# Kernel tuning notes

Hardware: AMD Instinct MI355X
Metric: run time of the kernel (lower is better)

The kernel has to match this reference:

```python
import jax, jax.numpy as jnp
import numpy as np

D_MODEL = 128
NUM_HEADS = 8
DEPTH = D_MODEL // NUM_HEADS
NEG = -1e9


def _dense_params(key, d_in, d_out):
    kw, kb = jax.random.split(key)
    # Glorot-uniform like keras Dense default
    lim = np.sqrt(6.0 / (d_in + d_out))
    w = jax.random.uniform(kw, (d_in, d_out), jnp.float32, -lim, lim)
    b = jnp.zeros((d_out,), jnp.float32)
    return w, b


def setup_inputs() -> dict:
    key = jax.random.key(0)
    ks = jax.random.split(key, 16)
    B, N, M, d = 256, 128, 128, D_MODEL
    inp = {
        'x_self': jax.random.normal(ks[0], (B, N, d), jnp.float32),
        'adj_self': jax.random.randint(ks[1], (B, N, N), 0, 2, jnp.int32),
        'mask_self': jnp.ones((B, N), jnp.int32),
        'x_cross': jax.random.normal(ks[2], (B, M, d), jnp.float32),
        'mask_cross': jnp.ones((B, M), jnp.int32),
    }
    names = ['wq_s', 'wk_s', 'wv_s', 'wo_s', 'wq_c', 'wk_c', 'wv_c', 'wo_c']
    for i, nm in enumerate(names):
        w, b = _dense_params(ks[3 + i], d, d)
        inp[nm] = w
        inp['b' + nm[1:]] = b
    wg, bg = _dense_params(ks[12], 3 * d, d)
    inp['wg'] = wg
    inp['bg'] = bg
    return inp


def _split_heads(x):
    B, N, _ = x.shape
    return x.reshape(B, N, NUM_HEADS, DEPTH).transpose(0, 2, 1, 3)  # [B,H,N,depth]


def _merge_heads(x):
    B, H, N, Dp = x.shape
    return x.transpose(0, 2, 1, 3).reshape(B, N, H * Dp)


def _attention(q, k, v, mask, adj=None):
    # q,k,v: [B,H,Nq,depth]; mask: [B,Nk]; adj: [B,Nq,Nk] or None
    logits = jnp.einsum('bhqd,bhkd->bhqk', q, k) / jnp.sqrt(jnp.float32(DEPTH))
    if adj is not None:
        logits = logits + ((1.0 - adj.astype(jnp.float32)) * NEG)[:, None, :, :]
    logits = logits + ((1.0 - mask.astype(jnp.float32)) * NEG)[:, None, None, :]
    w = jax.nn.softmax(logits, axis=-1)
    return jnp.einsum('bhqk,bhkd->bhqd', w, v)


def reference(x_self, adj_self, mask_self, x_cross, mask_cross,
              wq_s, bq_s, wk_s, bk_s, wv_s, bv_s, wo_s, bo_s,
              wq_c, bq_c, wk_c, bk_c, wv_c, bv_c, wo_c, bo_c,
              wg, bg):
    # Self attention (adjacency + padding mask)
    q_s = _split_heads(x_self @ wq_s + bq_s)
    k_s = _split_heads(x_self @ wk_s + bk_s)
    v_s = _split_heads(x_self @ wv_s + bv_s)
    out_s = _merge_heads(_attention(q_s, k_s, v_s, mask_self, adj_self)) @ wo_s + bo_s
    # Cross attention (padding mask only); dropout inactive at inference
    q_c = _split_heads(x_self @ wq_c + bq_c)
    k_c = _split_heads(x_cross @ wk_c + bk_c)
    v_c = _split_heads(x_cross @ wv_c + bv_c)
    out_c = _merge_heads(_attention(q_c, k_c, v_c, mask_cross)) @ wo_c + bo_c
    # Sigmoid gate fusion
    gate = jax.nn.sigmoid(jnp.concatenate([x_self, out_s, out_c], axis=-1) @ wg + bg)
    return (1.0 - gate) * out_s + gate * out_c
```

## Files before the change

kernel.cpp:

```cpp
#include <hip/hip_runtime.h>
#include <hip/hip_bf16.h>

typedef _Float16 f16_t;
typedef __attribute__((ext_vector_type(8))) _Float16 f16x8;
typedef __attribute__((ext_vector_type(4))) float f32x4;

__device__ __forceinline__ f16x8 cvt8(const float* p) {
  float4 v0 = *(const float4*)p;
  float4 v1 = *(const float4*)(p + 4);
  f16x8 a;
  a[0] = (f16_t)v0.x; a[1] = (f16_t)v0.y; a[2] = (f16_t)v0.z; a[3] = (f16_t)v0.w;
  a[4] = (f16_t)v1.x; a[5] = (f16_t)v1.y; a[6] = (f16_t)v1.z; a[7] = (f16_t)v1.w;
  return a;
}

__global__ __launch_bounds__(256) void prep_kernel(
    const float* wq_s, const float* wk_s, const float* wv_s,
    const float* wq_c, const float* wk_c, const float* wv_c,
    const float* wo_s, const float* wo_c, const float* wg,
    const float* bos, const float* boc, const float* bgin,
    f16_t* WT, float* bgp)
{
  const int b = blockIdx.x;
  const int tid = threadIdx.x;
  if (b < 11) {
    __shared__ float t[128][129];
    const float* src; f16_t* dst; int ostride;
    switch (b) {
      case 0: src = wq_s; break; case 1: src = wk_s; break;
      case 2: src = wv_s; break; case 3: src = wq_c; break;
      case 4: src = wk_c; break; case 5: src = wv_c; break;
      case 6: src = wo_s; break; case 7: src = wo_c; break;
      default: src = wg + (size_t)(b - 8) * 16384; break;
    }
    if (b < 8) { dst = WT + (size_t)b * 16384; ostride = 128; }
    else       { dst = WT + 8 * 16384 + (b - 8) * 128; ostride = 384; }
#pragma unroll
    for (int i = 0; i < 64; ++i) {
      const int idx = tid + i * 256;
      t[idx & 127][idx >> 7] = src[idx];
    }
    __syncthreads();
#pragma unroll
    for (int i = 0; i < 64; ++i) {
      const int idx = tid + i * 256;
      const int c = idx >> 7, r = idx & 127;
      dst[(size_t)c * ostride + r] = (f16_t)t[c][r];
    }
  } else if (b < 13) {
    const int matsel = b - 11;
    const float* wo = matsel ? wo_c : wo_s;
    const int joff = 128 + matsel * 128;
    f16_t* dst = WT + (size_t)(11 + matsel) * 16384;
    const int wv = tid >> 6, ln = tid & 63, l15 = ln & 15, g = ln >> 4;
    f32x4 acc[2][8];
#pragma unroll
    for (int mm = 0; mm < 2; ++mm)
#pragma unroll
      for (int nt = 0; nt < 8; ++nt) acc[mm][nt] = (f32x4){0.f, 0.f, 0.f, 0.f};
#pragma unroll
    for (int kt = 0; kt < 4; ++kt) {
      f16x8 a[2];
#pragma unroll
      for (int mm = 0; mm < 2; ++mm) {
        const int crow = wv * 32 + mm * 16 + l15;
#pragma unroll
        for (int jj = 0; jj < 8; ++jj)
          a[mm][jj] = (f16_t)wg[(size_t)(joff + kt * 32 + g * 8 + jj) * 128 + crow];
      }
#pragma unroll
      for (int nt = 0; nt < 8; ++nt) {
        f16x8 bf = cvt8(wo + (size_t)(nt * 16 + l15) * 128 + kt * 32 + g * 8);
        acc[0][nt] = __builtin_amdgcn_mfma_f32_16x16x32_f16(a[0], bf, acc[0][nt], 0, 0, 0);
        acc[1][nt] = __builtin_amdgcn_mfma_f32_16x16x32_f16(a[1], bf, acc[1][nt], 0, 0, 0);
      }
    }
#pragma unroll
    for (int mm = 0; mm < 2; ++mm)
#pragma unroll
      for (int nt = 0; nt < 8; ++nt)
#pragma unroll
        for (int r = 0; r < 4; ++r) {
          const int c = wv * 32 + mm * 16 + g * 4 + r;
          dst[(size_t)c * 128 + nt * 16 + l15] = (f16_t)acc[mm][nt][r];
        }
  } else {
    if (tid < 128) {
      float acc = bgin[tid];
      for (int j = 0; j < 128; ++j)
        acc += bos[j] * wg[(size_t)(128 + j) * 128 + tid] +
               boc[j] * wg[(size_t)(256 + j) * 128 + tid];
      bgp[tid] = acc;
    }
  }
}

template <bool TRANSP>
__device__ __forceinline__ void gemm4(
    const f16x8 afr[4], const f16_t* __restrict__ W, const float* __restrict__ bias,
    char* Ob, int l15, int g, int rg, int colbase)
{
  f32x4 acc[4];
#pragma unroll
  for (int nt = 0; nt < 4; ++nt) acc[nt] = (f32x4){0.f, 0.f, 0.f, 0.f};
#pragma unroll
  for (int nt = 0; nt < 4; ++nt)
#pragma unroll
    for (int kt = 0; kt < 4; ++kt) {
      f16x8 b = *(const f16x8*)(W + (size_t)(colbase + nt * 16 + l15) * 128 + kt * 32 + g * 8);
      acc[nt] = __builtin_amdgcn_mfma_f32_16x16x32_f16(afr[kt], b, acc[nt], 0, 0, 0);
    }
#pragma unroll
  for (int nt = 0; nt < 4; ++nt) {
    const int col = colbase + nt * 16 + l15;
    const float bv = bias[col];
#pragma unroll
    for (int r = 0; r < 4; ++r) {
      const int row = rg * 16 + g * 4 + r;
      const f16_t v = (f16_t)(acc[nt][r] + bv);
      if (TRANSP)
        *(f16_t*)(Ob + col * 256 + ((row * 2) ^ ((col & 7) << 4))) = v;
      else
        *(f16_t*)(Ob + row * 256 + ((col * 2) ^ ((row & 7) << 4))) = v;
    }
  }
}

__device__ __forceinline__ void gemmQ(
    const f16x8 afr[4], const f16_t* __restrict__ W, const float* __restrict__ bias,
    char* scr, int l15, int g, int colbase, f16x8 bq[4])
{
  f32x4 acc[4];
#pragma unroll
  for (int nt = 0; nt < 4; ++nt) acc[nt] = (f32x4){0.f, 0.f, 0.f, 0.f};
#pragma unroll
  for (int nt = 0; nt < 4; ++nt)
#pragma unroll
    for (int kt = 0; kt < 4; ++kt) {
      f16x8 b = *(const f16x8*)(W + (size_t)(colbase + nt * 16 + l15) * 128 + kt * 32 + g * 8);
      acc[nt] = __builtin_amdgcn_mfma_f32_16x16x32_f16(afr[kt], b, acc[nt], 0, 0, 0);
    }
#pragma unroll
  for (int nt = 0; nt < 4; ++nt) {
    const int col = colbase + nt * 16 + l15;
    const float bv = bias[col];
    const int dloc = nt * 16 + l15;
#pragma unroll
    for (int r = 0; r < 4; ++r) {
      const int qp = g * 4 + r;
      *(f16_t*)(scr + qp * 128 + ((dloc * 2) ^ ((qp & 7) << 4))) = (f16_t)(acc[nt][r] + bv);
    }
  }
#pragma unroll
  for (int h = 0; h < 4; ++h) {
    f16x8 z = {0, 0, 0, 0, 0, 0, 0, 0};
    bq[h] = (g < 2)
      ? *(const f16x8*)(scr + l15 * 128 + (((h * 16 + g * 8) * 2) ^ ((l15 & 7) << 4)))
      : z;
  }
}

__device__ __forceinline__ void attn_w(
    const char* Kb, const char* Vtb, char* ATTo, char* Pw,
    const f16x8 bq[4], const unsigned aw[4],
    int l15, int g, int rg, int ch)
{
  const f32x4 zero = (f32x4){0.f, 0.f, 0.f, 0.f};
  const int psw = (l15 & 3) << 4;
#pragma unroll
  for (int hp = 0; hp < 4; ++hp) {
    const int h = ch * 4 + hp;
    f32x4 st[8];
#pragma unroll
    for (int kt = 0; kt < 8; ++kt) {
      const int krow = kt * 16 + l15;
      f16x8 ak = {0, 0, 0, 0, 0, 0, 0, 0};
      if (g < 2)
        ak = *(const f16x8*)(Kb + krow * 256 + (((h * 16 + g * 8) * 2) ^ ((krow & 7) << 4)));
      st[kt] = __builtin_amdgcn_mfma_f32_16x16x32_f16(ak, bq[hp], zero, 0, 0, 0);
    }
    float psum = 0.f;
#pragma unroll
    for (int kt = 0; kt < 8; ++kt)
#pragma unroll
      for (int r = 0; r < 4; ++r) {
        const int k = kt * 16 + g * 4 + r;
        const float e = __expf(st[kt][r] * 0.25f - 8.f);
        const float p = ((aw[k >> 5] >> (k & 31)) & 1u) ? e : 0.f;
        st[kt][r] = p;
        psum += p;
      }
    psum += __shfl_xor(psum, 16);
    psum += __shfl_xor(psum, 32);
    const float inv = 1.f / psum;

    f32x4 o = zero;
#pragma unroll
    for (int qt = 0; qt < 4; ++qt) {
#pragma unroll
      for (int hf = 0; hf < 2; ++hf) {
        const int kt = qt * 2 + hf;
        union { f16_t hh[4]; unsigned long long u; } pk;
#pragma unroll
        for (int r = 0; r < 4; ++r) pk.hh[r] = (f16_t)(st[kt][r] * inv);
        *(unsigned long long*)(Pw + l15 * 64 + (((hf * 16 + g * 4) * 2) ^ psw)) = pk.u;
      }
      f16x8 pa = *(const f16x8*)(Pw + l15 * 64 + ((g * 16) ^ psw));
      const int d = h * 16 + l15;
      f16x8 vb = *(const f16x8*)(Vtb + d * 256 + (((qt * 32 + g * 8) * 2) ^ ((d & 7) << 4)));
      o = __builtin_amdgcn_mfma_f32_16x16x32_f16(pa, vb, o, 0, 0, 0);
    }
#pragma unroll
    for (int r = 0; r < 4; ++r) {
      const int row = rg * 16 + g * 4 + r;
      *(f16_t*)(ATTo + row * 256 + (((h * 16 + l15) * 2) ^ ((row & 7) << 4))) = (f16_t)o[r];
    }
  }
}

__global__ __launch_bounds__(1024, 4) void fused2_kernel(
    const float* __restrict__ Xs_g, const float* __restrict__ Xc_g,
    const int* __restrict__ adj, const int* __restrict__ mask_s,
    const int* __restrict__ mask_c, const f16_t* __restrict__ WT,
    const float* __restrict__ bq_s, const float* __restrict__ bk_s,
    const float* __restrict__ bv_s, const float* __restrict__ bq_c,
    const float* __restrict__ bk_c, const float* __restrict__ bv_c,
    const float* __restrict__ bos, const float* __restrict__ boc,
    const float* __restrict__ bgp, float* __restrict__ OUT)
{
  __shared__ __align__(16) char Kb[32768];
  __shared__ __align__(16) char Vtb[32768];
  __shared__ __align__(16) char ATTs[32768];
  __shared__ __align__(16) char ATTc[32768];
  __shared__ __align__(16) char PR[16384];
  __shared__ unsigned mwS[4], mwC[4];

  const int bb = blockIdx.x;
  const int tid = threadIdx.x;
  const int wv = tid >> 6, ln = tid & 63, l15 = ln & 15, g = ln >> 4;
  const int rg = wv & 7, ch = wv >> 3;
  const int colbase = ch * 64;
  const int arow = rg * 16 + l15;

  if (tid < 512) {
    const int r = tid >> 2, w = tid & 3;
    const int4* ap = (const int4*)(adj + (size_t)bb * 16384 + r * 128 + w * 32);
    unsigned bits = 0;
#pragma unroll
    for (int i = 0; i < 8; ++i) {
      int4 a = ap[i];
      bits |= ((a.x != 0 ? 1u : 0u) | (a.y != 0 ? 2u : 0u) |
               (a.z != 0 ? 4u : 0u) | (a.w != 0 ? 8u : 0u)) << (i * 4);
    }
    *(unsigned*)(ATTc + r * 16 + w * 4) = bits;
  }
  if (wv < 2) {
    unsigned long long bm = __ballot(mask_s[bb * 128 + wv * 64 + ln] != 0);
    if (ln == 0) { mwS[wv * 2] = (unsigned)bm; mwS[wv * 2 + 1] = (unsigned)(bm >> 32); }
  } else if (wv < 4) {
    unsigned long long bm = __ballot(mask_c[bb * 128 + (wv - 2) * 64 + ln] != 0);
    if (ln == 0) { mwC[(wv - 2) * 2] = (unsigned)bm; mwC[(wv - 2) * 2 + 1] = (unsigned)(bm >> 32); }
  }

  f16x8 bqs[4], bqc[4];
  {
    f16x8 afr[4];
#pragma unroll
    for (int kt = 0; kt < 4; ++kt)
      afr[kt] = cvt8(Xs_g + (size_t)bb * 16384 + arow * 128 + kt * 32 + g * 8);
    gemm4<false>(afr, WT + 1 * 16384, bk_s, Kb, l15, g, rg, colbase);
    gemm4<true >(afr, WT + 2 * 16384, bv_s, Vtb, l15, g, rg, colbase);
    char* scr = ATTs + wv * 2048;
    gemmQ(afr, WT + 0 * 16384, bq_s, scr, l15, g, colbase, bqs);
    gemmQ(afr, WT + 3 * 16384, bq_c, scr, l15, g, colbase, bqc);
  }
  __syncthreads();

  {
    const uint4 a4 = *(const uint4*)(ATTc + arow * 16);
    unsigned aw[4] = {a4.x & mwS[0], a4.y & mwS[1], a4.z & mwS[2], a4.w & mwS[3]};
    attn_w(Kb, Vtb, ATTs, PR + wv * 1024, bqs, aw, l15, g, rg, ch);
  }
  __syncthreads();

  {
    f16x8 afr[4];
#pragma unroll
    for (int kt = 0; kt < 4; ++kt)
      afr[kt] = cvt8(Xc_g + (size_t)bb * 16384 + arow * 128 + kt * 32 + g * 8);
    gemm4<false>(afr, WT + 4 * 16384, bk_c, Kb, l15, g, rg, colbase);
    gemm4<true >(afr, WT + 5 * 16384, bv_c, Vtb, l15, g, rg, colbase);
  }
  __syncthreads();

  {
    unsigned aw[4] = {mwC[0], mwC[1], mwC[2], mwC[3]};
    attn_w(Kb, Vtb, ATTc, PR + wv * 1024, bqc, aw, l15, g, rg, ch);
  }
  __syncthreads();

  {
    const int asw = (arow & 7) << 4;
    f16x8 aS[4], aC[4], aX[4];
#pragma unroll
    for (int kt = 0; kt < 4; ++kt) {
      aS[kt] = *(const f16x8*)(ATTs + arow * 256 + ((kt * 64 + g * 16) ^ asw));
      aC[kt] = *(const f16x8*)(ATTc + arow * 256 + ((kt * 64 + g * 16) ^ asw));
      aX[kt] = cvt8(Xs_g + (size_t)bb * 16384 + arow * 128 + kt * 32 + g * 8);
    }
    const f16_t* WoS = WT + 6 * 16384;
    const f16_t* WoC = WT + 7 * 16384;
    const f16_t* Wg1 = WT + 8 * 16384;
    const f16_t* W2p = WT + 11 * 16384;
    const f16_t* W3p = WT + 12 * 16384;
    f32x4 accS[4], accC[4], accG[4];
#pragma unroll
    for (int nt = 0; nt < 4; ++nt) {
      accS[nt] = (f32x4){0.f, 0.f, 0.f, 0.f};
      accC[nt] = (f32x4){0.f, 0.f, 0.f, 0.f};
      accG[nt] = (f32x4){0.f, 0.f, 0.f, 0.f};
    }
#pragma unroll
    for (int nt = 0; nt < 4; ++nt) {
      const size_t col = colbase + nt * 16 + l15;
#pragma unroll
      for (int kt = 0; kt < 4; ++kt) {
        const size_t ko = kt * 32 + g * 8;
        f16x8 bS = *(const f16x8*)(WoS + col * 128 + ko);
        f16x8 bC = *(const f16x8*)(WoC + col * 128 + ko);
        f16x8 bG = *(const f16x8*)(Wg1 + col * 384 + ko);
        f16x8 b2 = *(const f16x8*)(W2p + col * 128 + ko);
        f16x8 b3 = *(const f16x8*)(W3p + col * 128 + ko);
        accS[nt] = __builtin_amdgcn_mfma_f32_16x16x32_f16(aS[kt], bS, accS[nt], 0, 0, 0);
        accC[nt] = __builtin_amdgcn_mfma_f32_16x16x32_f16(aC[kt], bC, accC[nt], 0, 0, 0);
        accG[nt] = __builtin_amdgcn_mfma_f32_16x16x32_f16(aX[kt], bG, accG[nt], 0, 0, 0);
        accG[nt] = __builtin_amdgcn_mfma_f32_16x16x32_f16(aS[kt], b2, accG[nt], 0, 0, 0);
        accG[nt] = __builtin_amdgcn_mfma_f32_16x16x32_f16(aC[kt], b3, accG[nt], 0, 0, 0);
      }
    }
#pragma unroll
    for (int nt = 0; nt < 4; ++nt) {
      const int col = colbase + nt * 16 + l15;
      const float bS = bos[col], bC = boc[col], bG = bgp[col];
#pragma unroll
      for (int r = 0; r < 4; ++r) {
        const int row = rg * 16 + g * 4 + r;
        const float os = accS[nt][r] + bS;
        const float oc = accC[nt][r] + bC;
        const float gv = 1.f / (1.f + __expf(-(accG[nt][r] + bG)));
        OUT[(size_t)bb * 16384 + row * 128 + col] = (1.f - gv) * os + gv * oc;
      }
    }
  }
}

extern "C" void kernel_launch(void* const* d_in, const int* in_sizes, int n_in,
                              void* d_out, int out_size, void* d_ws, size_t ws_size,
                              hipStream_t stream)
{
  const float* x_self  = (const float*)d_in[0];
  const int*   adj     = (const int*)d_in[1];
  const int*   mask_s  = (const int*)d_in[2];
  const float* x_cross = (const float*)d_in[3];
  const int*   mask_c  = (const int*)d_in[4];
  const float* wq_s = (const float*)d_in[5];
  const float* bq_s = (const float*)d_in[6];
  const float* wk_s = (const float*)d_in[7];
  const float* bk_s = (const float*)d_in[8];
  const float* wv_s = (const float*)d_in[9];
  const float* bv_s = (const float*)d_in[10];
  const float* wo_s = (const float*)d_in[11];
  const float* bo_s = (const float*)d_in[12];
  const float* wq_c = (const float*)d_in[13];
  const float* bq_c = (const float*)d_in[14];
  const float* wk_c = (const float*)d_in[15];
  const float* bk_c = (const float*)d_in[16];
  const float* wv_c = (const float*)d_in[17];
  const float* bv_c = (const float*)d_in[18];
  const float* wo_c = (const float*)d_in[19];
  const float* bo_c = (const float*)d_in[20];
  const float* wg   = (const float*)d_in[21];
  const float* bg   = (const float*)d_in[22];
  float* out = (float*)d_out;

  f16_t* WT  = (f16_t*)d_ws;
  float* bgp = (float*)(WT + 13 * 16384);

  prep_kernel<<<14, 256, 0, stream>>>(wq_s, wk_s, wv_s, wq_c, wk_c, wv_c,
                                      wo_s, wo_c, wg, bo_s, bo_c, bg, WT, bgp);
  fused2_kernel<<<256, 1024, 0, stream>>>(x_self, x_cross, adj, mask_s, mask_c, WT,
                                          bq_s, bk_s, bv_s, bq_c, bk_c, bv_c,
                                          bo_s, bo_c, bgp, out);
}
```

Baseline: 143.1 us.

## Stream softmax chunks into PV MFMA with deferred normalization, prefetch cross inputs

The attention routine now computes QK scores two tiles at a time and converts them to probabilities right away. Each chunk goes into the PV MFMA immediately, and the 1/sum normalization is applied to the output via a lane shuffle. This avoids holding all eight score tiles in registers. The P scratch changes from an XOR swizzle to a padded 80-byte row stride, and compiler memory fences are inserted. X_cross fragments are also loaded at kernel start and the min-waves launch bound is dropped, which raises register pressure and may lower occupancy.

```diff
diff --git a/kernel.cpp b/kernel.cpp
--- a/kernel.cpp
+++ b/kernel.cpp
@@ -4,6 +4,8 @@
 typedef _Float16 f16_t;
 typedef __attribute__((ext_vector_type(8))) _Float16 f16x8;
 typedef __attribute__((ext_vector_type(4))) float f32x4;
+
+#define LFENCE() asm volatile("" ::: "memory")
 
 __device__ __forceinline__ f16x8 cvt8(const float* p) {
   float4 v0 = *(const float4*)p;
@@ -130,6 +132,7 @@
     const f16x8 afr[4], const f16_t* __restrict__ W, const float* __restrict__ bias,
     char* scr, int l15, int g, int colbase, f16x8 bq[4])
 {
+  LFENCE();
   f32x4 acc[4];
 #pragma unroll
   for (int nt = 0; nt < 4; ++nt) acc[nt] = (f32x4){0.f, 0.f, 0.f, 0.f};
@@ -151,6 +154,7 @@
       *(f16_t*)(scr + qp * 128 + ((dloc * 2) ^ ((qp & 7) << 4))) = (f16_t)(acc[nt][r] + bv);
     }
   }
+  LFENCE();
 #pragma unroll
   for (int h = 0; h < 4; ++h) {
     f16x8 z = {0, 0, 0, 0, 0, 0, 0, 0};
@@ -158,6 +162,7 @@
       ? *(const f16x8*)(scr + l15 * 128 + (((h * 16 + g * 8) * 2) ^ ((l15 & 7) << 4)))
       : z;
   }
+  LFENCE();
 }
 
 __device__ __forceinline__ void attn_w(
@@ -166,59 +171,58 @@
     int l15, int g, int rg, int ch)
 {
   const f32x4 zero = (f32x4){0.f, 0.f, 0.f, 0.f};
-  const int psw = (l15 & 3) << 4;
 #pragma unroll
   for (int hp = 0; hp < 4; ++hp) {
     const int h = ch * 4 + hp;
-    f32x4 st[8];
-#pragma unroll
-    for (int kt = 0; kt < 8; ++kt) {
-      const int krow = kt * 16 + l15;
-      f16x8 ak = {0, 0, 0, 0, 0, 0, 0, 0};
-      if (g < 2)
-        ak = *(const f16x8*)(Kb + krow * 256 + (((h * 16 + g * 8) * 2) ^ ((krow & 7) << 4)));
-      st[kt] = __builtin_amdgcn_mfma_f32_16x16x32_f16(ak, bq[hp], zero, 0, 0, 0);
-    }
+    const int d = h * 16 + l15;
     float psum = 0.f;
-#pragma unroll
-    for (int kt = 0; kt < 8; ++kt)
-#pragma unroll
-      for (int r = 0; r < 4; ++r) {
-        const int k = kt * 16 + g * 4 + r;
-        const float e = __expf(st[kt][r] * 0.25f - 8.f);
-        const float p = ((aw[k >> 5] >> (k & 31)) & 1u) ? e : 0.f;
-        st[kt][r] = p;
-        psum += p;
-      }
+    f32x4 o = zero;
+#pragma unroll
+    for (int c = 0; c < 4; ++c) {
+      f32x4 st[2];
+#pragma unroll
+      for (int hf = 0; hf < 2; ++hf) {
+        const int krow = (c * 2 + hf) * 16 + l15;
+        f16x8 ak = {0, 0, 0, 0, 0, 0, 0, 0};
+        if (g < 2)
+          ak = *(const f16x8*)(Kb + krow * 256 + (((h * 16 + g * 8) * 2) ^ ((krow & 7) << 4)));
+        st[hf] = __builtin_amdgcn_mfma_f32_16x16x32_f16(ak, bq[hp], zero, 0, 0, 0);
+      }
+#pragma unroll
+      for (int hf = 0; hf < 2; ++hf) {
+        union { f16_t hh[4]; unsigned long long u; } pk;
+#pragma unroll
+        for (int r = 0; r < 4; ++r) {
+          const int k = (c * 2 + hf) * 16 + g * 4 + r;
+          const float e = __expf(st[hf][r] * 0.25f - 4.f);
+          const float p = ((aw[k >> 5] >> (k & 31)) & 1u) ? e : 0.f;
+          psum += p;
+          pk.hh[r] = (f16_t)p;
+        }
+        *(unsigned long long*)(Pw + l15 * 80 + hf * 32 + g * 8) = pk.u;
+      }
+      LFENCE();
+      union { unsigned long long u[2]; f16x8 v; } pa2;
+      pa2.u[0] = *(const unsigned long long*)(Pw + l15 * 80 + g * 16);
+      pa2.u[1] = *(const unsigned long long*)(Pw + l15 * 80 + g * 16 + 8);
+      LFENCE();
+      f16x8 vb = *(const f16x8*)(Vtb + d * 256 + (((c * 32 + g * 8) * 2) ^ ((d & 7) << 4)));
+      o = __builtin_amdgcn_mfma_f32_16x16x32_f16(pa2.v, vb, o, 0, 0, 0);
+    }
     psum += __shfl_xor(psum, 16);
     psum += __shfl_xor(psum, 32);
     const float inv = 1.f / psum;
-
-    f32x4 o = zero;
-#pragma unroll
-    for (int qt = 0; qt < 4; ++qt) {
-#pragma unroll
-      for (int hf = 0; hf < 2; ++hf) {
-        const int kt = qt * 2 + hf;
-        union { f16_t hh[4]; unsigned long long u; } pk;
-#pragma unroll
-        for (int r = 0; r < 4; ++r) pk.hh[r] = (f16_t)(st[kt][r] * inv);
-        *(unsigned long long*)(Pw + l15 * 64 + (((hf * 16 + g * 4) * 2) ^ psw)) = pk.u;
-      }
-      f16x8 pa = *(const f16x8*)(Pw + l15 * 64 + ((g * 16) ^ psw));
-      const int d = h * 16 + l15;
-      f16x8 vb = *(const f16x8*)(Vtb + d * 256 + (((qt * 32 + g * 8) * 2) ^ ((d & 7) << 4)));
-      o = __builtin_amdgcn_mfma_f32_16x16x32_f16(pa, vb, o, 0, 0, 0);
-    }
 #pragma unroll
     for (int r = 0; r < 4; ++r) {
+      const float invq = __shfl(inv, g * 4 + r);
       const int row = rg * 16 + g * 4 + r;
-      *(f16_t*)(ATTo + row * 256 + (((h * 16 + l15) * 2) ^ ((row & 7) << 4))) = (f16_t)o[r];
-    }
-  }
-}
-
-__global__ __launch_bounds__(1024, 4) void fused2_kernel(
+      *(f16_t*)(ATTo + row * 256 + (((h * 16 + l15) * 2) ^ ((row & 7) << 4))) =
+          (f16_t)(o[r] * invq);
+    }
+  }
+}
+
+__global__ __launch_bounds__(1024) void fused5_kernel(
     const float* __restrict__ Xs_g, const float* __restrict__ Xc_g,
     const int* __restrict__ adj, const int* __restrict__ mask_s,
     const int* __restrict__ mask_c, const f16_t* __restrict__ WT,
@@ -232,7 +236,7 @@
   __shared__ __align__(16) char Vtb[32768];
   __shared__ __align__(16) char ATTs[32768];
   __shared__ __align__(16) char ATTc[32768];
-  __shared__ __align__(16) char PR[16384];
+  __shared__ __align__(16) char PR[20480];
   __shared__ unsigned mwS[4], mwC[4];
 
   const int bb = blockIdx.x;
@@ -262,12 +266,15 @@
     if (ln == 0) { mwC[(wv - 2) * 2] = (unsigned)bm; mwC[(wv - 2) * 2 + 1] = (unsigned)(bm >> 32); }
   }
 
-  f16x8 bqs[4], bqc[4];
+  f16x8 bqs[4], bqc[4], afrc[4];
   {
     f16x8 afr[4];
 #pragma unroll
     for (int kt = 0; kt < 4; ++kt)
       afr[kt] = cvt8(Xs_g + (size_t)bb * 16384 + arow * 128 + kt * 32 + g * 8);
+#pragma unroll
+    for (int kt = 0; kt < 4; ++kt)
+      afrc[kt] = cvt8(Xc_g + (size_t)bb * 16384 + arow * 128 + kt * 32 + g * 8);
     gemm4<false>(afr, WT + 1 * 16384, bk_s, Kb, l15, g, rg, colbase);
     gemm4<true >(afr, WT + 2 * 16384, bv_s, Vtb, l15, g, rg, colbase);
     char* scr = ATTs + wv * 2048;
@@ -279,23 +286,19 @@
   {
     const uint4 a4 = *(const uint4*)(ATTc + arow * 16);
     unsigned aw[4] = {a4.x & mwS[0], a4.y & mwS[1], a4.z & mwS[2], a4.w & mwS[3]};
-    attn_w(Kb, Vtb, ATTs, PR + wv * 1024, bqs, aw, l15, g, rg, ch);
+    attn_w(Kb, Vtb, ATTs, PR + wv * 1280, bqs, aw, l15, g, rg, ch);
   }
   __syncthreads();
 
   {
-    f16x8 afr[4];
-#pragma unroll
-    for (int kt = 0; kt < 4; ++kt)
-      afr[kt] = cvt8(Xc_g + (size_t)bb * 16384 + arow * 128 + kt * 32 + g * 8);
-    gemm4<false>(afr, WT + 4 * 16384, bk_c, Kb, l15, g, rg, colbase);
-    gemm4<true >(afr, WT + 5 * 16384, bv_c, Vtb, l15, g, rg, colbase);
+    gemm4<false>(afrc, WT + 4 * 16384, bk_c, Kb, l15, g, rg, colbase);
+    gemm4<true >(afrc, WT + 5 * 16384, bv_c, Vtb, l15, g, rg, colbase);
   }
   __syncthreads();
 
   {
     unsigned aw[4] = {mwC[0], mwC[1], mwC[2], mwC[3]};
-    attn_w(Kb, Vtb, ATTc, PR + wv * 1024, bqc, aw, l15, g, rg, ch);
+    attn_w(Kb, Vtb, ATTc, PR + wv * 1280, bqc, aw, l15, g, rg, ch);
   }
   __syncthreads();
 
@@ -388,7 +391,7 @@
 
   prep_kernel<<<14, 256, 0, stream>>>(wq_s, wk_s, wv_s, wq_c, wk_c, wv_c,
                                       wo_s, wo_c, wg, bo_s, bo_c, bg, WT, bgp);
-  fused2_kernel<<<256, 1024, 0, stream>>>(x_self, x_cross, adj, mask_s, mask_c, WT,
+  fused5_kernel<<<256, 1024, 0, stream>>>(x_self, x_cross, adj, mask_s, mask_c, WT,
                                           bq_s, bk_s, bv_s, bq_c, bk_c, bv_c,
                                           bo_s, bo_c, bgp, out);
 }
```

Result: no change. 144.8 us (+1.2%).
